# Optimization experiments

Hardware: AMD Instinct MI355X
Metric: run time of the kernel (lower is better)

Reference implementation:

```python
import jax, jax.numpy as jnp
import numpy as np

B, N, C, R, E = 8, 4096, 128, 16, 65536


def setup_inputs() -> dict:
    key = jax.random.key(0)
    ks = jax.random.split(key, 8)
    node_features = jax.random.normal(ks[0], (B, N, C), dtype=jnp.float32)
    edge_index = jax.random.randint(ks[1], (B, 2, E), 0, N, dtype=jnp.int64)
    edge_type = jax.random.randint(ks[2], (B, E), 0, R, dtype=jnp.int64)
    s = 1.0 / np.sqrt(C)
    rel_weight = jax.random.uniform(ks[3], (R, C, C), jnp.float32, -s, s)
    root_weight = jax.random.uniform(ks[4], (C, C), jnp.float32, -s, s)
    rgcn_bias = jnp.zeros((C,), jnp.float32)
    lin_weight = jax.random.uniform(ks[5], (C, 1), jnp.float32, -s, s)
    lin_bias = jnp.zeros((1,), jnp.float32)
    return {
        'node_features': node_features,
        'edge_index': edge_index,
        'edge_type': edge_type,
        'rel_weight': rel_weight,
        'root_weight': root_weight,
        'rgcn_bias': rgcn_bias,
        'lin_weight': lin_weight,
        'lin_bias': lin_bias,
    }


def _rgcn_score(node_features, edge_index, edge_type, rel_weight, root_weight,
                rgcn_bias, lin_weight, lin_bias):
    # Flatten batch of graphs into one big disjoint graph (as batch_rgcn does).
    x = node_features.reshape(B * N, C)
    offs = (jnp.arange(B, dtype=edge_index.dtype) * N)[:, None, None]  # (B,1,1)
    ei = (edge_index + offs).transpose(1, 0, 2).reshape(2, B * E)  # (2, B*E)
    et = edge_type.reshape(B * E)
    src, dst = ei[0], ei[1]

    x_src = x[src]  # (B*E, C) gathered source features
    # root transform + bias (RGCNConv root_weight + bias)
    out = x @ root_weight + rgcn_bias  # (B*N, C)
    # per-relation mean aggregation; mean(W_r x_j) == W_r mean(x_j)
    for r in range(R):
        mask = (et == r).astype(x.dtype)  # (B*E,)
        s = jax.ops.segment_sum(x_src * mask[:, None], dst, num_segments=B * N)
        cnt = jax.ops.segment_sum(mask, dst, num_segments=B * N)
        mean = jnp.where(cnt[:, None] > 0, s / jnp.maximum(cnt, 1.0)[:, None], 0.0)
        out = out + mean @ rel_weight[r]

    out = jax.nn.relu(out)  # dropout is identity at eval
    scores = (out @ lin_weight + lin_bias).reshape(B, N)
    return scores


def reference(node_features, edge_index, edge_type, rel_weight, root_weight,
              rgcn_bias, lin_weight, lin_bias):
    return _rgcn_score(node_features, edge_index, edge_type, rel_weight,
                       root_weight, rgcn_bias, lin_weight, lin_bias)
```

## Files before the change

kernel.cpp:

```cpp
#include <hip/hip_runtime.h>

#define BB 8
#define NN 4096
#define CC 128
#define RR 16
#define EE 65536
#define NNODES 32768
#define NEDGES 524288
#define BCAP  48
#define SCE   15
#define NT    16
#define ALP   136

typedef unsigned short ushort_t;
typedef short bf16x8 __attribute__((ext_vector_type(8)));
typedef float f32x4 __attribute__((ext_vector_type(4)));

__device__ __forceinline__ unsigned short f2b(float f) {
    unsigned u = __builtin_bit_cast(unsigned, f);
    unsigned r = (u + 0x7fffu + ((u >> 16) & 1u)) >> 16;
    return (unsigned short)r;
}
__device__ __forceinline__ float b2f(unsigned short s) {
    return __builtin_bit_cast(float, (unsigned)s << 16);
}
__device__ __forceinline__ float ldf(const void* p, int j, int isbf) {
    return isbf ? b2f(((const ushort_t*)p)[j]) : ((const float*)p)[j];
}
__device__ __forceinline__ int ldi(const int* p, int j, int is64) {
    return p[j << is64];
}
__device__ __forceinline__ unsigned cvtpk(float lo, float hi) {
    unsigned r;
    asm("v_cvt_pk_bf16_f32 %0, %1, %2" : "=v"(r) : "v"(lo), "v"(hi));
    return r;
}

#define GSUM8(u) do { \
    s[0] += __builtin_bit_cast(float, (u).x << 16); \
    s[1] += __builtin_bit_cast(float, (u).x & 0xffff0000u); \
    s[2] += __builtin_bit_cast(float, (u).y << 16); \
    s[3] += __builtin_bit_cast(float, (u).y & 0xffff0000u); \
    s[4] += __builtin_bit_cast(float, (u).z << 16); \
    s[5] += __builtin_bit_cast(float, (u).z & 0xffff0000u); \
    s[6] += __builtin_bit_cast(float, (u).w << 16); \
    s[7] += __builtin_bit_cast(float, (u).w & 0xffff0000u); \
} while (0)

__global__ __launch_bounds__(256) void prep_k(const void* __restrict__ x,
                                              const void* __restrict__ relw,
                                              const void* __restrict__ rootw,
                                              const int* __restrict__ ei,
                                              const int* __restrict__ et,
                                              ushort_t* __restrict__ Xb,
                                              ushort_t* __restrict__ WT3,
                                              int* __restrict__ dcnt,
                                              int* __restrict__ bucket,
                                              int isbf, int w64i, int w64t) {
    int bx = blockIdx.x, t = threadIdx.x;
    if (bx < 1024) {
        int b = bx & 7;
        #pragma unroll
        for (int i = 0; i < 2; ++i) {
            int e = (bx >> 3) * 512 + i * 256 + t;
            int src = ldi(ei, (b * 2) * EE + e, w64i);
            int dst = ldi(ei, (b * 2 + 1) * EE + e, w64i);
            int r = ldi(et, (b << 16) + e, w64t);
            int gd = (b << 12) + dst;
            int pos = atomicAdd(&dcnt[gd << 4], 1);
            if (pos < BCAP)
                bucket[gd * BCAP + pos] = (((b << 12) + src) << 4) | r;
        }
    } else if (bx < 1536) {
        int bx2 = bx - 1024;
        int base = (bx2 & 7) * 65536 + (bx2 >> 3) * 256 + t;
        #pragma unroll
        for (int i = 0; i < 4; ++i) {
            int tid = base + i * 16384;
            if (isbf) {
                ((uint4*)Xb)[tid] = ((const uint4*)x)[tid];
            } else {
                const float4* xf = (const float4*)x;
                float4 a = xf[2 * tid], b = xf[2 * tid + 1];
                ushort4 o0, o1;
                o0.x = f2b(a.x); o0.y = f2b(a.y); o0.z = f2b(a.z); o0.w = f2b(a.w);
                o1.x = f2b(b.x); o1.y = f2b(b.y); o1.z = f2b(b.z); o1.w = f2b(b.w);
                ((ushort4*)Xb)[2 * tid] = o0; ((ushort4*)Xb)[2 * tid + 1] = o1;
            }
        }
    } else {
        __shared__ ushort_t Ls[128 * 40];
        int mb = bx - 1536;
        int mat = mb >> 2, chunk = mb & 3;
        const void* src = (mat == 16) ? rootw : relw;
        int soff = (mat == 16) ? 0 : mat * 16384;
        int k0 = chunk * 32;
        #pragma unroll
        for (int i = 0; i < 16; ++i) {
            int idx = t + i * 256;
            int k = idx >> 7, c = idx & 127;
            Ls[c * 40 + k] = f2b(ldf(src, soff + (k0 + k) * 128 + c, isbf));
        }
        __syncthreads();
        #pragma unroll
        for (int i = 0; i < 2; ++i) {
            int idx = t + i * 256;
            int cg = idx >> 6, lane = idx & 63;
            int lrow = lane & 15, lq = lane >> 4;
            uint4 v = *(const uint4*)(&Ls[(cg * 16 + lrow) * 40 + lq * 8]);
            *(uint4*)(WT3 + ((size_t)((mat * 4 + chunk) * 8 + cg)) * 512 + lane * 8) = v;
        }
    }
}

__global__ __launch_bounds__(256, 6) void agg_k(const ushort_t* __restrict__ Xb,
                                                const ushort_t* __restrict__ WT3,
                                                const int* __restrict__ dcnt,
                                                const int* __restrict__ bucket,
                                                const void* __restrict__ bias,
                                                const void* __restrict__ linw,
                                                const void* __restrict__ linb,
                                                void* __restrict__ out,
                                                int isbf) {
    __shared__ int scnt[NT * 16];
    __shared__ ushort_t srt[NT * 16 * 16];
    __shared__ ushort_t A[2][NT * ALP];
    __shared__ float red[NT][5];
    int bx = blockIdx.x, t = threadIdx.x;
    int n0 = (bx & 7) * NN + (bx >> 3) * NT;

    scnt[t] = 0;
    __syncthreads();

    int nsub = t >> 4, tsub = t & 15;
    int gn = n0 + nsub;
    int offA = tsub * 8;
    int nc = dcnt[gn << 4]; if (nc > BCAP) nc = BCAP;
    const int* bk = bucket + gn * BCAP;
    for (int j = tsub; j < nc; j += 16) {
        int v = bk[j];
        int row = (nsub << 4) + (v & 15);
        int pos = atomicAdd(&scnt[row], 1);
        if (pos < SCE)
            srt[(row << 4) + 1 + pos] = (ushort_t)((unsigned)v >> 4);
    }
    __syncthreads();
    srt[t << 4] = (ushort_t)scnt[t];
    __syncthreads();

    int wave = t >> 6, lane = t & 63, lrow = lane & 15, lq = lane >> 4;
    f32x4 acc0 = {}, acc1 = {};

    {
        int row = nsub << 4;
        uint4 q0 = *(const uint4*)(&srt[row << 4]);
        int cf = q0.x & 0xffffu; int ce = cf > SCE ? SCE : cf;
        float s[8];
        #pragma unroll
        for (int j = 0; j < 8; ++j) s[j] = 0.f;
        for (int e = 0; e < ce; ++e) {
            int gs = srt[(row << 4) + 1 + e];
            uint4 u = *(const uint4*)(Xb + (size_t)gs * 128 + offA);
            GSUM8(u);
        }
        float w = (cf > 0) ? 1.0f / (float)cf : 0.f;
        uint4 va;
        va.x = cvtpk(s[0] * w, s[1] * w); va.y = cvtpk(s[2] * w, s[3] * w);
        va.z = cvtpk(s[4] * w, s[5] * w); va.w = cvtpk(s[6] * w, s[7] * w);
        *(uint4*)(&A[0][nsub * ALP + offA]) = va;
    }
    __syncthreads();

    for (int p = 0; p < 17; ++p) {
        int np = p + 1;
        uint4 r0, r1, r2, r3;
        int cf = 0, ce = 0, row = 0;
        if (np < 16) {
            row = (nsub << 4) + np;
            uint4 q0 = *(const uint4*)(&srt[row << 4]);
            cf = q0.x & 0xffffu; ce = cf > SCE ? SCE : cf;
            int e0 = q0.x >> 16, e1 = q0.y & 0xffffu, e2 = q0.y >> 16, e3 = q0.z & 0xffffu;
            if (ce > 0) r0 = *(const uint4*)(Xb + (size_t)e0 * 128 + offA);
            if (ce > 1) r1 = *(const uint4*)(Xb + (size_t)e1 * 128 + offA);
            if (ce > 2) r2 = *(const uint4*)(Xb + (size_t)e2 * 128 + offA);
            if (ce > 3) r3 = *(const uint4*)(Xb + (size_t)e3 * 128 + offA);
        } else if (np == 16) {
            r0 = *(const uint4*)(Xb + (size_t)gn * 128 + offA);
        }
        const ushort_t* Ap = A[p & 1];
        const ushort_t* bw = WT3 + (size_t)p * 16384 + (wave * 2) * 512 + lane * 8;
        __builtin_amdgcn_s_setprio(1);
        #pragma unroll
        for (int ks = 0; ks < 4; ++ks) {
            int k0 = ks * 32 + lq * 8;
            bf16x8 a0 = *(const bf16x8*)(&Ap[lrow * ALP + k0]);
            bf16x8 b0 = *(const bf16x8*)(bw + ks * 4096);
            bf16x8 b1 = *(const bf16x8*)(bw + ks * 4096 + 512);
            acc0 = __builtin_amdgcn_mfma_f32_16x16x32_bf16(a0, b0, acc0, 0, 0, 0);
            acc1 = __builtin_amdgcn_mfma_f32_16x16x32_bf16(a0, b1, acc1, 0, 0, 0);
        }
        __builtin_amdgcn_s_setprio(0);
        if (np < 16) {
            float s[8];
            #pragma unroll
            for (int j = 0; j < 8; ++j) s[j] = 0.f;
            if (ce > 0) GSUM8(r0);
            if (ce > 1) GSUM8(r1);
            if (ce > 2) GSUM8(r2);
            if (ce > 3) GSUM8(r3);
            if (ce > 4) {
                for (int e4 = 4; e4 < ce; ++e4) {
                    int gs = srt[(row << 4) + 1 + e4];
                    uint4 u = *(const uint4*)(Xb + (size_t)gs * 128 + offA);
                    GSUM8(u);
                }
            }
            float w = (cf > 0) ? 1.0f / (float)cf : 0.f;
            uint4 va;
            va.x = cvtpk(s[0] * w, s[1] * w); va.y = cvtpk(s[2] * w, s[3] * w);
            va.z = cvtpk(s[4] * w, s[5] * w); va.w = cvtpk(s[6] * w, s[7] * w);
            *(uint4*)(&A[np & 1][nsub * ALP + offA]) = va;
        } else if (np == 16) {
            *(uint4*)(&A[np & 1][nsub * ALP + offA]) = r0;
        }
        if (p < 16) __syncthreads();
    }

    int wn = wave << 5;
    int c0 = wn + lrow, c1 = wn + 16 + lrow;
    float bi0 = ldf(bias, c0, isbf), bi1 = ldf(bias, c1, isbf);
    float lw0 = ldf(linw, c0, isbf), lw1 = ldf(linw, c1, isbf);
    #pragma unroll
    for (int rg = 0; rg < 4; ++rg) {
        float p = fmaxf(acc0[rg] + bi0, 0.f) * lw0
                + fmaxf(acc1[rg] + bi1, 0.f) * lw1;
        p += __shfl_xor(p, 1, 64);
        p += __shfl_xor(p, 2, 64);
        p += __shfl_xor(p, 4, 64);
        p += __shfl_xor(p, 8, 64);
        if (lrow == 0) red[lq * 4 + rg][wave] = p;
    }
    __syncthreads();
    if (t < NT) {
        float res = red[t][0] + red[t][1] + red[t][2] + red[t][3] + ldf(linb, 0, isbf);
        if (isbf) ((ushort_t*)out)[n0 + t] = f2b(res);
        else      ((float*)out)[n0 + t] = res;
    }
}

extern "C" void kernel_launch(void* const* d_in, const int* in_sizes, int n_in,
                              void* d_out, int out_size, void* d_ws, size_t ws_size,
                              hipStream_t stream) {
    const void* x     = d_in[0];
    const int*  ei    = (const int*)d_in[1];
    const int*  et    = (const int*)d_in[2];
    const void* relw  = d_in[3];
    const void* rootw = d_in[4];
    const void* bias  = d_in[5];
    const void* linw  = d_in[6];
    const void* linb  = d_in[7];

    int isbf = (in_sizes[0] == BB * NN * CC * 2);
    int w64i = (in_sizes[1] == BB * 2 * EE * 8);
    int w64t = (in_sizes[2] == BB * EE * 8);

    const size_t WS_NEED = 17334272;
    if (ws_size < WS_NEED) return;

    char* ws = (char*)d_ws;
    ushort_t* Xb     = (ushort_t*)(ws);
    ushort_t* WT3    = (ushort_t*)(ws + 8388608);
    int*      dcnt   = (int*)(ws + 8945664);
    int*      bucket = (int*)(ws + 11042816);

    hipMemsetAsync(dcnt, 0, 2097152, stream);
    prep_k<<<1604, 256, 0, stream>>>(x, relw, rootw, ei, et, Xb, WT3, dcnt, bucket,
                                     isbf, w64i, w64t);
    agg_k<<<2048, 256, 0, stream>>>(Xb, WT3, dcnt, bucket, bias, linw, linb, d_out, isbf);
}
```

Baseline: 163.4 us.

## Process 32 nodes per block to halve weight-tile loads and use packed f32 adds

Doubles the node tile per block from 16 to 32, so each wave issues four MFMAs per k-step and every weight fragment loaded from global serves twice as many rows, with half as many blocks. Each thread now gathers two 8-element chunks per edge, and the bf16 accumulation uses 2-wide float vectors so the compiler can emit packed adds. The double-buffered A tile becomes a single buffer with an extra barrier per relation, which removes the overlap between the MFMAs and the writes of the next aggregation. Occupancy hint drops from 6 to 5 and the grid is halved.

```diff
diff --git a/kernel.cpp b/kernel.cpp
--- a/kernel.cpp
+++ b/kernel.cpp
@@ -9,12 +9,13 @@
 #define NEDGES 524288
 #define BCAP  48
 #define SCE   15
-#define NT    16
+#define NT    32
 #define ALP   136
 
 typedef unsigned short ushort_t;
 typedef short bf16x8 __attribute__((ext_vector_type(8)));
 typedef float f32x4 __attribute__((ext_vector_type(4)));
+typedef float f32x2 __attribute__((ext_vector_type(2)));
 
 __device__ __forceinline__ unsigned short f2b(float f) {
     unsigned u = __builtin_bit_cast(unsigned, f);
@@ -35,16 +36,19 @@
     asm("v_cvt_pk_bf16_f32 %0, %1, %2" : "=v"(r) : "v"(lo), "v"(hi));
     return r;
 }
-
-#define GSUM8(u) do { \
-    s[0] += __builtin_bit_cast(float, (u).x << 16); \
-    s[1] += __builtin_bit_cast(float, (u).x & 0xffff0000u); \
-    s[2] += __builtin_bit_cast(float, (u).y << 16); \
-    s[3] += __builtin_bit_cast(float, (u).y & 0xffff0000u); \
-    s[4] += __builtin_bit_cast(float, (u).z << 16); \
-    s[5] += __builtin_bit_cast(float, (u).z & 0xffff0000u); \
-    s[6] += __builtin_bit_cast(float, (u).w << 16); \
-    s[7] += __builtin_bit_cast(float, (u).w & 0xffff0000u); \
+__device__ __forceinline__ float bcf(unsigned u) { return __builtin_bit_cast(float, u); }
+
+#define GSUM8P(u) do { \
+    s2[0] += (f32x2){bcf((u).x << 16), bcf((u).x & 0xffff0000u)}; \
+    s2[1] += (f32x2){bcf((u).y << 16), bcf((u).y & 0xffff0000u)}; \
+    s2[2] += (f32x2){bcf((u).z << 16), bcf((u).z & 0xffff0000u)}; \
+    s2[3] += (f32x2){bcf((u).w << 16), bcf((u).w & 0xffff0000u)}; \
+} while (0)
+#define GSUM8P2(u) do { \
+    s2[4] += (f32x2){bcf((u).x << 16), bcf((u).x & 0xffff0000u)}; \
+    s2[5] += (f32x2){bcf((u).y << 16), bcf((u).y & 0xffff0000u)}; \
+    s2[6] += (f32x2){bcf((u).z << 16), bcf((u).z & 0xffff0000u)}; \
+    s2[7] += (f32x2){bcf((u).w << 16), bcf((u).w & 0xffff0000u)}; \
 } while (0)
 
 __global__ __launch_bounds__(256) void prep_k(const void* __restrict__ x,
@@ -113,7 +117,7 @@
     }
 }
 
-__global__ __launch_bounds__(256, 6) void agg_k(const ushort_t* __restrict__ Xb,
+__global__ __launch_bounds__(256, 5) void agg_k(const ushort_t* __restrict__ Xb,
                                                 const ushort_t* __restrict__ WT3,
                                                 const int* __restrict__ dcnt,
                                                 const int* __restrict__ bucket,
@@ -124,20 +128,20 @@
                                                 int isbf) {
     __shared__ int scnt[NT * 16];
     __shared__ ushort_t srt[NT * 16 * 16];
-    __shared__ ushort_t A[2][NT * ALP];
+    __shared__ ushort_t A[NT * ALP];
     __shared__ float red[NT][5];
     int bx = blockIdx.x, t = threadIdx.x;
     int n0 = (bx & 7) * NN + (bx >> 3) * NT;
 
-    scnt[t] = 0;
-    __syncthreads();
-
-    int nsub = t >> 4, tsub = t & 15;
+    scnt[t] = 0; scnt[256 + t] = 0;
+    __syncthreads();
+
+    int nsub = t >> 3, tsub = t & 7;
     int gn = n0 + nsub;
-    int offA = tsub * 8;
+    int offA = tsub * 8, offB = 64 + tsub * 8;
     int nc = dcnt[gn << 4]; if (nc > BCAP) nc = BCAP;
     const int* bk = bucket + gn * BCAP;
-    for (int j = tsub; j < nc; j += 16) {
+    for (int j = tsub; j < nc; j += 8) {
         int v = bk[j];
         int row = (nsub << 4) + (v & 15);
         int pos = atomicAdd(&scnt[row], 1);
@@ -146,84 +150,101 @@
     }
     __syncthreads();
     srt[t << 4] = (ushort_t)scnt[t];
+    srt[(t + 256) << 4] = (ushort_t)scnt[t + 256];
     __syncthreads();
 
     int wave = t >> 6, lane = t & 63, lrow = lane & 15, lq = lane >> 4;
-    f32x4 acc0 = {}, acc1 = {};
+    f32x4 acc[2][2] = {};
 
     {
         int row = nsub << 4;
         uint4 q0 = *(const uint4*)(&srt[row << 4]);
         int cf = q0.x & 0xffffu; int ce = cf > SCE ? SCE : cf;
-        float s[8];
-        #pragma unroll
-        for (int j = 0; j < 8; ++j) s[j] = 0.f;
+        f32x2 s2[8] = {};
         for (int e = 0; e < ce; ++e) {
             int gs = srt[(row << 4) + 1 + e];
-            uint4 u = *(const uint4*)(Xb + (size_t)gs * 128 + offA);
-            GSUM8(u);
-        }
-        float w = (cf > 0) ? 1.0f / (float)cf : 0.f;
-        uint4 va;
-        va.x = cvtpk(s[0] * w, s[1] * w); va.y = cvtpk(s[2] * w, s[3] * w);
-        va.z = cvtpk(s[4] * w, s[5] * w); va.w = cvtpk(s[6] * w, s[7] * w);
-        *(uint4*)(&A[0][nsub * ALP + offA]) = va;
+            const ushort_t* xr = Xb + (size_t)gs * 128;
+            uint4 ua = *(const uint4*)(xr + offA), ub = *(const uint4*)(xr + offB);
+            GSUM8P(ua); GSUM8P2(ub);
+        }
+        f32x2 w2 = {0.f, 0.f};
+        if (cf > 0) { float w = 1.0f / (float)cf; w2 = (f32x2){w, w}; }
+        #pragma unroll
+        for (int j = 0; j < 8; ++j) s2[j] *= w2;
+        uint4 va, vb;
+        va.x = cvtpk(s2[0].x, s2[0].y); va.y = cvtpk(s2[1].x, s2[1].y);
+        va.z = cvtpk(s2[2].x, s2[2].y); va.w = cvtpk(s2[3].x, s2[3].y);
+        vb.x = cvtpk(s2[4].x, s2[4].y); vb.y = cvtpk(s2[5].x, s2[5].y);
+        vb.z = cvtpk(s2[6].x, s2[6].y); vb.w = cvtpk(s2[7].x, s2[7].y);
+        *(uint4*)(&A[nsub * ALP + offA]) = va;
+        *(uint4*)(&A[nsub * ALP + offB]) = vb;
     }
     __syncthreads();
 
     for (int p = 0; p < 17; ++p) {
         int np = p + 1;
-        uint4 r0, r1, r2, r3;
+        uint4 r0a, r0b, r1a, r1b, r2a, r2b, r3a, r3b;
         int cf = 0, ce = 0, row = 0;
         if (np < 16) {
             row = (nsub << 4) + np;
             uint4 q0 = *(const uint4*)(&srt[row << 4]);
             cf = q0.x & 0xffffu; ce = cf > SCE ? SCE : cf;
             int e0 = q0.x >> 16, e1 = q0.y & 0xffffu, e2 = q0.y >> 16, e3 = q0.z & 0xffffu;
-            if (ce > 0) r0 = *(const uint4*)(Xb + (size_t)e0 * 128 + offA);
-            if (ce > 1) r1 = *(const uint4*)(Xb + (size_t)e1 * 128 + offA);
-            if (ce > 2) r2 = *(const uint4*)(Xb + (size_t)e2 * 128 + offA);
-            if (ce > 3) r3 = *(const uint4*)(Xb + (size_t)e3 * 128 + offA);
+            if (ce > 0) { const ushort_t* xr = Xb + (size_t)e0 * 128; r0a = *(const uint4*)(xr + offA); r0b = *(const uint4*)(xr + offB); }
+            if (ce > 1) { const ushort_t* xr = Xb + (size_t)e1 * 128; r1a = *(const uint4*)(xr + offA); r1b = *(const uint4*)(xr + offB); }
+            if (ce > 2) { const ushort_t* xr = Xb + (size_t)e2 * 128; r2a = *(const uint4*)(xr + offA); r2b = *(const uint4*)(xr + offB); }
+            if (ce > 3) { const ushort_t* xr = Xb + (size_t)e3 * 128; r3a = *(const uint4*)(xr + offA); r3b = *(const uint4*)(xr + offB); }
         } else if (np == 16) {
-            r0 = *(const uint4*)(Xb + (size_t)gn * 128 + offA);
-        }
-        const ushort_t* Ap = A[p & 1];
+            const ushort_t* xr = Xb + (size_t)gn * 128;
+            r0a = *(const uint4*)(xr + offA); r0b = *(const uint4*)(xr + offB);
+        }
         const ushort_t* bw = WT3 + (size_t)p * 16384 + (wave * 2) * 512 + lane * 8;
         __builtin_amdgcn_s_setprio(1);
         #pragma unroll
         for (int ks = 0; ks < 4; ++ks) {
             int k0 = ks * 32 + lq * 8;
-            bf16x8 a0 = *(const bf16x8*)(&Ap[lrow * ALP + k0]);
+            bf16x8 a0 = *(const bf16x8*)(&A[lrow * ALP + k0]);
+            bf16x8 a1 = *(const bf16x8*)(&A[(16 + lrow) * ALP + k0]);
             bf16x8 b0 = *(const bf16x8*)(bw + ks * 4096);
             bf16x8 b1 = *(const bf16x8*)(bw + ks * 4096 + 512);
-            acc0 = __builtin_amdgcn_mfma_f32_16x16x32_bf16(a0, b0, acc0, 0, 0, 0);
-            acc1 = __builtin_amdgcn_mfma_f32_16x16x32_bf16(a0, b1, acc1, 0, 0, 0);
+            acc[0][0] = __builtin_amdgcn_mfma_f32_16x16x32_bf16(a0, b0, acc[0][0], 0, 0, 0);
+            acc[0][1] = __builtin_amdgcn_mfma_f32_16x16x32_bf16(a0, b1, acc[0][1], 0, 0, 0);
+            acc[1][0] = __builtin_amdgcn_mfma_f32_16x16x32_bf16(a1, b0, acc[1][0], 0, 0, 0);
+            acc[1][1] = __builtin_amdgcn_mfma_f32_16x16x32_bf16(a1, b1, acc[1][1], 0, 0, 0);
         }
         __builtin_amdgcn_s_setprio(0);
+        if (p == 16) break;
+        __syncthreads();
         if (np < 16) {
-            float s[8];
-            #pragma unroll
-            for (int j = 0; j < 8; ++j) s[j] = 0.f;
-            if (ce > 0) GSUM8(r0);
-            if (ce > 1) GSUM8(r1);
-            if (ce > 2) GSUM8(r2);
-            if (ce > 3) GSUM8(r3);
+            f32x2 s2[8] = {};
+            if (ce > 0) { GSUM8P(r0a); GSUM8P2(r0b); }
+            if (ce > 1) { GSUM8P(r1a); GSUM8P2(r1b); }
+            if (ce > 2) { GSUM8P(r2a); GSUM8P2(r2b); }
+            if (ce > 3) { GSUM8P(r3a); GSUM8P2(r3b); }
             if (ce > 4) {
                 for (int e4 = 4; e4 < ce; ++e4) {
                     int gs = srt[(row << 4) + 1 + e4];
-                    uint4 u = *(const uint4*)(Xb + (size_t)gs * 128 + offA);
-                    GSUM8(u);
+                    const ushort_t* xr = Xb + (size_t)gs * 128;
+                    uint4 ta = *(const uint4*)(xr + offA), tb = *(const uint4*)(xr + offB);
+                    GSUM8P(ta); GSUM8P2(tb);
                 }
             }
-            float w = (cf > 0) ? 1.0f / (float)cf : 0.f;
-            uint4 va;
-            va.x = cvtpk(s[0] * w, s[1] * w); va.y = cvtpk(s[2] * w, s[3] * w);
-            va.z = cvtpk(s[4] * w, s[5] * w); va.w = cvtpk(s[6] * w, s[7] * w);
-            *(uint4*)(&A[np & 1][nsub * ALP + offA]) = va;
-        } else if (np == 16) {
-            *(uint4*)(&A[np & 1][nsub * ALP + offA]) = r0;
-        }
-        if (p < 16) __syncthreads();
+            f32x2 w2 = {0.f, 0.f};
+            if (cf > 0) { float w = 1.0f / (float)cf; w2 = (f32x2){w, w}; }
+            #pragma unroll
+            for (int j = 0; j < 8; ++j) s2[j] *= w2;
+            uint4 va, vb;
+            va.x = cvtpk(s2[0].x, s2[0].y); va.y = cvtpk(s2[1].x, s2[1].y);
+            va.z = cvtpk(s2[2].x, s2[2].y); va.w = cvtpk(s2[3].x, s2[3].y);
+            vb.x = cvtpk(s2[4].x, s2[4].y); vb.y = cvtpk(s2[5].x, s2[5].y);
+            vb.z = cvtpk(s2[6].x, s2[6].y); vb.w = cvtpk(s2[7].x, s2[7].y);
+            *(uint4*)(&A[nsub * ALP + offA]) = va;
+            *(uint4*)(&A[nsub * ALP + offB]) = vb;
+        } else {
+            *(uint4*)(&A[nsub * ALP + offA]) = r0a;
+            *(uint4*)(&A[nsub * ALP + offB]) = r0b;
+        }
+        __syncthreads();
     }
 
     int wn = wave << 5;
@@ -231,15 +252,17 @@
     float bi0 = ldf(bias, c0, isbf), bi1 = ldf(bias, c1, isbf);
     float lw0 = ldf(linw, c0, isbf), lw1 = ldf(linw, c1, isbf);
     #pragma unroll
-    for (int rg = 0; rg < 4; ++rg) {
-        float p = fmaxf(acc0[rg] + bi0, 0.f) * lw0
-                + fmaxf(acc1[rg] + bi1, 0.f) * lw1;
-        p += __shfl_xor(p, 1, 64);
-        p += __shfl_xor(p, 2, 64);
-        p += __shfl_xor(p, 4, 64);
-        p += __shfl_xor(p, 8, 64);
-        if (lrow == 0) red[lq * 4 + rg][wave] = p;
-    }
+    for (int mi = 0; mi < 2; ++mi)
+        #pragma unroll
+        for (int rg = 0; rg < 4; ++rg) {
+            float p = fmaxf(acc[mi][0][rg] + bi0, 0.f) * lw0
+                    + fmaxf(acc[mi][1][rg] + bi1, 0.f) * lw1;
+            p += __shfl_xor(p, 1, 64);
+            p += __shfl_xor(p, 2, 64);
+            p += __shfl_xor(p, 4, 64);
+            p += __shfl_xor(p, 8, 64);
+            if (lrow == 0) red[mi * 16 + lq * 4 + rg][wave] = p;
+        }
     __syncthreads();
     if (t < NT) {
         float res = red[t][0] + red[t][1] + red[t][2] + red[t][3] + ldf(linb, 0, isbf);
@@ -276,5 +299,5 @@
     hipMemsetAsync(dcnt, 0, 2097152, stream);
     prep_k<<<1604, 256, 0, stream>>>(x, relw, rootw, ei, et, Xb, WT3, dcnt, bucket,
                                      isbf, w64i, w64t);
-    agg_k<<<2048, 256, 0, stream>>>(Xb, WT3, dcnt, bucket, bias, linw, linb, d_out, isbf);
-}
+    agg_k<<<1024, 256, 0, stream>>>(Xb, WT3, dcnt, bucket, bias, linw, linb, d_out, isbf);
+}
```

Result: faster. 151.8 us (-7.1%).
